# Optimization experiments

Measured on AMD Instinct MI355X. Metric: run time of the kernel, lower is better.

Reference implementation:

```python
import jax, jax.numpy as jnp
import numpy as np

B, VD, SD, CD, H, HEADS = 16384, 2048, 1024, 512, 256, 4
DH = H // HEADS
EPS = 1e-5


def layer_norm(x, g, b):
    m = jnp.mean(x, axis=-1, keepdims=True)
    v = jnp.var(x, axis=-1, keepdims=True)
    return (x - m) * jax.lax.rsqrt(v + EPS) * g + b


def setup_inputs() -> dict:
    key = jax.random.key(0)
    ks = jax.random.split(key, 16)
    sc = 0.02
    inp = {
        'fv': jax.random.normal(ks[0], (B, VD), jnp.float32),
        'fs': jax.random.normal(ks[1], (B, SD), jnp.float32),
        'fc': jax.random.normal(ks[2], (B, CD), jnp.float32),
        # projection linears + layernorms
        'Wv': jax.random.normal(ks[3], (H, VD), jnp.float32) * sc,
        'bv': jnp.zeros((H,), jnp.float32),
        'gv': jnp.ones((H,), jnp.float32), 'bev': jnp.zeros((H,), jnp.float32),
        'Ws': jax.random.normal(ks[4], (H, SD), jnp.float32) * sc,
        'bs': jnp.zeros((H,), jnp.float32),
        'gs': jnp.ones((H,), jnp.float32), 'bes': jnp.zeros((H,), jnp.float32),
        'Wc': jax.random.normal(ks[5], (H, CD), jnp.float32) * sc,
        'bc': jnp.zeros((H,), jnp.float32),
        'gc_': jnp.ones((H,), jnp.float32), 'bec': jnp.zeros((H,), jnp.float32),
        # MultiheadAttention packed in-proj and out-proj
        'in_w': jax.random.normal(ks[6], (3 * H, H), jnp.float32) * sc,
        'in_b': jnp.zeros((3 * H,), jnp.float32),
        'out_w': jax.random.normal(ks[7], (H, H), jnp.float32) * sc,
        'out_b': jnp.zeros((H,), jnp.float32),
        # post-attention layernorm
        'gn': jnp.ones((H,), jnp.float32), 'gb': jnp.zeros((H,), jnp.float32),
        # gating MLP: Linear(3H,64) -> GELU -> Linear(64,3) -> softmax
        'g1w': jax.random.normal(ks[8], (64, 3 * H), jnp.float32) * sc,
        'g1b': jnp.zeros((64,), jnp.float32),
        'g2w': jax.random.normal(ks[9], (3, 64), jnp.float32) * sc,
        'g2b': jnp.zeros((3,), jnp.float32),
    }
    return inp


def reference(fv, fs, fc, Wv, bv, gv, bev, Ws, bs, gs, bes, Wc, bc, gc_, bec,
              in_w, in_b, out_w, out_b, gn, gb, g1w, g1b, g2w, g2b):
    v = layer_norm(fv @ Wv.T + bv, gv, bev)   # [B,H]
    s = layer_norm(fs @ Ws.T + bs, gs, bes)
    c = layer_norm(fc @ Wc.T + bc, gc_, bec)
    stack = jnp.stack([v, s, c], axis=1)      # [B,3,H]

    # self-attention over seq=3 (eval mode: dropout off)
    qkv = stack @ in_w.T + in_b               # [B,3,3H]
    q, k, vv = jnp.split(qkv, 3, axis=-1)
    def heads(x):  # [B,3,H] -> [B,HEADS,3,DH]
        return x.reshape(B, 3, HEADS, DH).transpose(0, 2, 1, 3)
    q, k, vv = heads(q), heads(k), heads(vv)
    scores = jnp.einsum('bhqd,bhkd->bhqk', q, k) / jnp.sqrt(jnp.float32(DH))
    attn = jax.nn.softmax(scores, axis=-1)
    ctx = jnp.einsum('bhqk,bhkd->bhqd', attn, vv)
    ctx = ctx.transpose(0, 2, 1, 3).reshape(B, 3, H)
    attended = ctx @ out_w.T + out_b          # [B,3,H]

    attended = layer_norm(attended + stack, gn, gb)
    av, as_, ac = attended[:, 0], attended[:, 1], attended[:, 2]

    h1 = jax.nn.gelu(jnp.concatenate([av, as_, ac], axis=-1) @ g1w.T + g1b, approximate=False)
    gates = jax.nn.softmax(h1 @ g2w.T + g2b, axis=-1)  # [B,3]

    fused = gates[:, 0:1] * av + gates[:, 1:2] * as_ + gates[:, 2:3] * ac
    return (fused, gates)
```

## Files before the change

### kernel.cpp

```cpp
#include <hip/hip_runtime.h>
#include <math.h>


typedef unsigned short u16;
typedef __bf16 bf16x8 __attribute__((ext_vector_type(8)));
typedef float fx4 __attribute__((ext_vector_type(4)));

#define MFMA_BF16(A_, B_, C_) __builtin_amdgcn_mfma_f32_16x16x32_bf16((A_), (B_), (C_), 0, 0, 0)
#define WAIT_VM(N) asm volatile("s_waitcnt vmcnt(" #N ")" ::: "memory")

__device__ __forceinline__ float bf2f(u16 s) {
    union { float f; unsigned u; } c; c.u = ((unsigned)s) << 16; return c.f;
}
__device__ __forceinline__ u16 f2bf(float f) {
    union { float f; unsigned u; } c; c.f = f;
    return (u16)((c.u + 0x7fffu + ((c.u >> 16) & 1u)) >> 16);
}
__device__ __forceinline__ float bfpair_dot(unsigned a, unsigned b) {
    union { unsigned u; float f; } al, ah, bl, bh;
    al.u = a << 16; ah.u = a & 0xffff0000u;
    bl.u = b << 16; bh.u = b & 0xffff0000u;
    return al.f * bl.f + ah.f * bh.f;
}
__device__ __forceinline__ void gld16(void* l, const void* g) {
    __builtin_amdgcn_global_load_lds((const __attribute__((address_space(1))) void*)g,
                                     (__attribute__((address_space(3))) void*)l, 16, 0, 0);
}

__global__ __launch_bounds__(256) void cvt_w(const float* Wv, const float* Ws, const float* Wc,
                                             const float* inw, const float* outw, const float* g1w,
                                             u16* dst) {
    int idx = blockIdx.x * 256 + threadIdx.x;
    const float* src; int rel;
    if      (idx <  524288) { src = Wv;   rel = idx; }
    else if (idx <  786432) { src = Ws;   rel = idx -  524288; }
    else if (idx <  917504) { src = Wc;   rel = idx -  786432; }
    else if (idx < 1114112) { src = inw;  rel = idx -  917504; }
    else if (idx < 1179648) { src = outw; rel = idx - 1114112; }
    else                    { src = g1w;  rel = idx - 1179648; }
    dst[idx] = f2bf(src[rel]);
}

__global__ __launch_bounds__(256, 2) void gemm_ln(
    const float* fv, const float* fs, const float* fc,
    const u16* wWv, const u16* wWs, const u16* wWc,
    const float* bv, const float* gv, const float* bev,
    const float* bs, const float* gs, const float* bes,
    const float* bc, const float* gc_, const float* bec,
    u16* stack) {
    __shared__ alignas(16) char smem[76288];
    u16* sC = (u16*)smem;
    float* redS = (float*)(smem + 73728);
    float* redQ = (float*)(smem + 74752);
    float* mvS  = (float*)(smem + 75776);

    int bid = blockIdx.x;
    int slot, mblk;
    if (bid < 256)      { slot = 0; mblk = bid; }
    else if (bid < 512) { slot = 1; mblk = bid - 256; }
    else                { slot = 2; mblk = bid - 512; }

    const float* A; const u16* W; const float* bias; const float* gg; const float* be; int K;
    if (slot == 0)      { A = fv; W = wWv; bias = bv; gg = gv;  be = bev; K = 2048; }
    else if (slot == 1) { A = fs; W = wWs; bias = bs; gg = gs;  be = bes; K = 1024; }
    else                { A = fc; W = wWc; bias = bc; gg = gc_; be = bec; K = 512;  }

    int t = threadIdx.x, wv = t >> 6, ln = t & 63, q = ln >> 4, l15 = ln & 15;
    int m0 = mblk * 64;

    fx4 zero = {0.f, 0.f, 0.f, 0.f};
    fx4 acc[4][4];
    #pragma unroll
    for (int mi = 0; mi < 4; ++mi)
        #pragma unroll
        for (int ni = 0; ni < 4; ++ni) acc[mi][ni] = zero;

    int aR[2], aGC[2];
    #pragma unroll
    for (int i = 0; i < 2; ++i) {
        int d = wv * 128 + i * 64 + ln;
        aR[i] = d >> 3;
        aGC[i] = (d & 7) ^ (aR[i] & 7);
    }
    int bN[4], bKc[4];
    #pragma unroll
    for (int i = 0; i < 4; ++i) {
        int d = wv * 256 + i * 64 + ln;
        bN[i] = d >> 2;
        bKc[i] = (d & 3) ^ ((bN[i] >> 1) & 3);
    }

#define LN_ISSUE(ktile, bufoff)                                                   \
    {                                                                             \
        char* bA_ = smem + (bufoff);                                              \
        char* bB_ = bA_ + 8192;                                                   \
        _Pragma("unroll")                                                         \
        for (int i_ = 0; i_ < 2; ++i_)                                            \
            gld16(bA_ + (wv * 128 + i_ * 64) * 16,                                \
                  A + (size_t)(m0 + aR[i_]) * K + (ktile) * 32 + aGC[i_] * 4);    \
        _Pragma("unroll")                                                         \
        for (int i_ = 0; i_ < 4; ++i_)                                            \
            gld16(bB_ + (wv * 256 + i_ * 64) * 16,                                \
                  W + (size_t)bN[i_] * K + (ktile) * 32 + bKc[i_] * 8);           \
    }

    int niter = K >> 5;
    LN_ISSUE(0, 0);
    LN_ISSUE(1, 24576);
    int cb = 0;
    for (int kt = 0; kt < niter; ++kt) {
        if (kt + 1 < niter) { WAIT_VM(6); } else { WAIT_VM(0); }
        __builtin_amdgcn_sched_barrier(0);
        __builtin_amdgcn_s_barrier();
        __builtin_amdgcn_sched_barrier(0);
        int nb = cb + 2; if (nb >= 3) nb -= 3;
        if (kt + 2 < niter) LN_ISSUE(kt + 2, nb * 24576);

        const float* sAc = (const float*)(smem + cb * 24576);
        const u16*  sBc  = (const u16*)(smem + cb * 24576 + 8192);
        bf16x8 af[4], bfr[4];
        #pragma unroll
        for (int mi = 0; mi < 4; ++mi) {
            int r = mi * 16 + l15, s = r & 7;
            const float* rowp = sAc + r * 32;
            float4 c0 = *(const float4*)(rowp + ((2 * q) ^ s) * 4);
            float4 c1 = *(const float4*)(rowp + ((2 * q + 1) ^ s) * 4);
            af[mi][0] = (__bf16)c0.x; af[mi][1] = (__bf16)c0.y;
            af[mi][2] = (__bf16)c0.z; af[mi][3] = (__bf16)c0.w;
            af[mi][4] = (__bf16)c1.x; af[mi][5] = (__bf16)c1.y;
            af[mi][6] = (__bf16)c1.z; af[mi][7] = (__bf16)c1.w;
        }
        #pragma unroll
        for (int ni = 0; ni < 4; ++ni) {
            int n = wv * 64 + ni * 16 + l15;
            int ch = n * 4 + (q ^ ((n >> 1) & 3));
            bfr[ni] = *(const bf16x8*)(sBc + ch * 8);
        }
        __builtin_amdgcn_s_setprio(1);
        #pragma unroll
        for (int mi = 0; mi < 4; ++mi)
            #pragma unroll
            for (int ni = 0; ni < 4; ++ni)
                acc[mi][ni] = MFMA_BF16(af[mi], bfr[ni], acc[mi][ni]);
        __builtin_amdgcn_s_setprio(0);
        cb += 1; if (cb >= 3) cb -= 3;
    }
#undef LN_ISSUE

    float biasv[4], gvv[4], bevv[4];
    #pragma unroll
    for (int ni = 0; ni < 4; ++ni) {
        int col = wv * 64 + ni * 16 + l15;
        biasv[ni] = bias[col]; gvv[ni] = gg[col]; bevv[ni] = be[col];
    }
    #pragma unroll
    for (int mi = 0; mi < 4; ++mi)
        #pragma unroll
        for (int ni = 0; ni < 4; ++ni)
            #pragma unroll
            for (int r = 0; r < 4; ++r) acc[mi][ni][r] += biasv[ni];
    #pragma unroll
    for (int mi = 0; mi < 4; ++mi) {
        #pragma unroll
        for (int r = 0; r < 4; ++r) {
            float s = 0.f, qq = 0.f;
            #pragma unroll
            for (int ni = 0; ni < 4; ++ni) { float x = acc[mi][ni][r]; s += x; qq += x * x; }
            #pragma unroll
            for (int m = 1; m < 16; m <<= 1) { s += __shfl_xor(s, m, 64); qq += __shfl_xor(qq, m, 64); }
            if (l15 == 0) { int rho = mi * 16 + q * 4 + r; redS[rho * 4 + wv] = s; redQ[rho * 4 + wv] = qq; }
        }
    }
    __syncthreads();
    if (t < 64) {
        float s = redS[t * 4] + redS[t * 4 + 1] + redS[t * 4 + 2] + redS[t * 4 + 3];
        float qq = redQ[t * 4] + redQ[t * 4 + 1] + redQ[t * 4 + 2] + redQ[t * 4 + 3];
        float mean = s * (1.f / 256.f);
        float var = qq * (1.f / 256.f) - mean * mean;
        mvS[t * 2] = mean; mvS[t * 2 + 1] = rsqrtf(var + 1e-5f);
    }
    __syncthreads();
    #pragma unroll
    for (int mi = 0; mi < 4; ++mi) {
        #pragma unroll
        for (int r = 0; r < 4; ++r) {
            int rho = mi * 16 + q * 4 + r;
            float mean = mvS[rho * 2], rstd = mvS[rho * 2 + 1];
            #pragma unroll
            for (int ni = 0; ni < 4; ++ni) {
                int col = wv * 64 + ni * 16 + l15;
                float x = (acc[mi][ni][r] - mean) * rstd * gvv[ni] + bevv[ni];
                sC[rho * 256 + col] = f2bf(x);
            }
        }
    }
    __syncthreads();
    u16* outp = stack + (size_t)m0 * 768 + slot * 256;
    #pragma unroll
    for (int it = 0; it < 8; ++it) {
        int idx = t + it * 256;
        int row = idx >> 5, c = idx & 31;
        uint4 v = *(const uint4*)(sC + row * 256 + c * 8);
        *(uint4*)(outp + (size_t)row * 768 + c * 8) = v;
    }
}

__global__ __launch_bounds__(256, 3) void gemm_qkv(const u16* stack, const u16* W, const float* in_b,
                                                   u16* qkv) {
    __shared__ alignas(16) char smem[49152];
    u16* sC = (u16*)smem;

    int t = threadIdx.x, wv = t >> 6, ln = t & 63, q = ln >> 4, l15 = ln & 15;
    int n0 = blockIdx.x * 128, m0 = blockIdx.y * 128;
    int wr = wv >> 1, wc = wv & 1;

    fx4 zero = {0.f, 0.f, 0.f, 0.f};
    fx4 acc[4][4];
    #pragma unroll
    for (int mi = 0; mi < 4; ++mi)
        #pragma unroll
        for (int ni = 0; ni < 4; ++ni) acc[mi][ni] = zero;

    int sR[2], sKc[2];
    #pragma unroll
    for (int i = 0; i < 2; ++i) {
        int d = wv * 128 + i * 64 + ln;
        sR[i] = d >> 2;
        sKc[i] = (d & 3) ^ ((sR[i] >> 1) & 3);
    }

#define QK_ISSUE(ktile, bufoff)                                                         \
    {                                                                                   \
        char* bA_ = smem + (bufoff);                                                    \
        char* bB_ = bA_ + 8192;                                                         \
        _Pragma("unroll")                                                               \
        for (int i_ = 0; i_ < 2; ++i_) {                                                \
            gld16(bA_ + (wv * 128 + i_ * 64) * 16,                                      \
                  stack + (size_t)(m0 + sR[i_]) * 256 + (ktile) * 32 + sKc[i_] * 8);    \
            gld16(bB_ + (wv * 128 + i_ * 64) * 16,                                      \
                  W + (size_t)(n0 + sR[i_]) * 256 + (ktile) * 32 + sKc[i_] * 8);        \
        }                                                                               \
    }

    QK_ISSUE(0, 0);
    QK_ISSUE(1, 16384);
    int cb = 0;
    for (int kt = 0; kt < 8; ++kt) {
        if (kt < 7) { WAIT_VM(4); } else { WAIT_VM(0); }
        __builtin_amdgcn_sched_barrier(0);
        __builtin_amdgcn_s_barrier();
        __builtin_amdgcn_sched_barrier(0);
        int nb = cb + 2; if (nb >= 3) nb -= 3;
        if (kt + 2 < 8) QK_ISSUE(kt + 2, nb * 16384);

        const u16* sAc = (const u16*)(smem + cb * 16384);
        const u16* sBc = (const u16*)(smem + cb * 16384 + 8192);
        bf16x8 af[4], bfr[4];
        #pragma unroll
        for (int mi = 0; mi < 4; ++mi) {
            int r = wr * 64 + mi * 16 + l15;
            int ch = r * 4 + (q ^ ((r >> 1) & 3));
            af[mi] = *(const bf16x8*)(sAc + ch * 8);
        }
        #pragma unroll
        for (int ni = 0; ni < 4; ++ni) {
            int n = wc * 64 + ni * 16 + l15;
            int ch = n * 4 + (q ^ ((n >> 1) & 3));
            bfr[ni] = *(const bf16x8*)(sBc + ch * 8);
        }
        __builtin_amdgcn_s_setprio(1);
        #pragma unroll
        for (int mi = 0; mi < 4; ++mi)
            #pragma unroll
            for (int ni = 0; ni < 4; ++ni)
                acc[mi][ni] = MFMA_BF16(af[mi], bfr[ni], acc[mi][ni]);
        __builtin_amdgcn_s_setprio(0);
        cb += 1; if (cb >= 3) cb -= 3;
    }
#undef QK_ISSUE
    __syncthreads();

    float biasv[4];
    #pragma unroll
    for (int ni = 0; ni < 4; ++ni) biasv[ni] = in_b[n0 + wc * 64 + ni * 16 + l15];
    #pragma unroll
    for (int mi = 0; mi < 4; ++mi)
        #pragma unroll
        for (int ni = 0; ni < 4; ++ni)
            #pragma unroll
            for (int r = 0; r < 4; ++r) {
                int rl = wr * 64 + mi * 16 + q * 4 + r;
                int cl = wc * 64 + ni * 16 + l15;
                sC[rl * 128 + cl] = f2bf(acc[mi][ni][r] + biasv[ni]);
            }
    __syncthreads();
    #pragma unroll
    for (int it = 0; it < 8; ++it) {
        int idx = t + it * 256;
        int row = idx >> 4, c = idx & 15;
        uint4 v = *(const uint4*)(sC + row * 128 + c * 8);
        *(uint4*)(qkv + (size_t)(m0 + row) * 768 + n0 + c * 8) = v;
    }
}

__global__ __launch_bounds__(256) void attn_k(const u16* qkv, u16* ctx) {
    __shared__ alignas(16) char smem[38016];
    u16* qs = (u16*)smem;
    float* sS = (float*)(smem + 36864);

    int t = threadIdx.x, wv = t >> 6, ln = t & 63;
    size_t base = (size_t)blockIdx.x * 8 * 2304;
    #pragma unroll
    for (int i = 0; i < 9; ++i) {
        int d = wv * 576 + i * 64;
        gld16((char*)smem + (size_t)d * 16, qkv + base + (size_t)(d + ln) * 8);
    }
    __syncthreads();
    #pragma unroll
    for (int it = 0; it < 2; ++it) {
        int idx = t + it * 256;
        if (idx < 288) {
            int b = idx / 36, rem = idx % 36, h = rem / 9, pp = rem % 9, i = pp / 3, j = pp % 3;
            const u16* qp = qs + b * 2304 + i * 768 + h * 64;
            const u16* kp = qs + b * 2304 + j * 768 + 256 + h * 64;
            float acc = 0.f;
            #pragma unroll
            for (int c = 0; c < 8; ++c) {
                uint4 qa = *(const uint4*)(qp + c * 8);
                uint4 ka = *(const uint4*)(kp + c * 8);
                acc += bfpair_dot(qa.x, ka.x) + bfpair_dot(qa.y, ka.y) +
                       bfpair_dot(qa.z, ka.z) + bfpair_dot(qa.w, ka.w);
            }
            sS[idx] = acc * 0.125f;
        }
    }
    __syncthreads();
    if (t < 96) {
        int b3 = t * 3;
        float s0 = sS[b3], s1 = sS[b3 + 1], s2 = sS[b3 + 2];
        float m = fmaxf(s0, fmaxf(s1, s2));
        float e0 = __expf(s0 - m), e1 = __expf(s1 - m), e2 = __expf(s2 - m);
        float inv = 1.f / (e0 + e1 + e2);
        sS[b3] = e0 * inv; sS[b3 + 1] = e1 * inv; sS[b3 + 2] = e2 * inv;
    }
    __syncthreads();
    #pragma unroll
    for (int it = 0; it < 3; ++it) {
        int idx = t + it * 256;
        int b = idx / 96, rem = idx % 96, i = rem / 32, c = rem & 31, h = c >> 3;
        int pbase = b * 36 + h * 9 + i * 3;
        float o[8];
        #pragma unroll
        for (int e = 0; e < 8; ++e) o[e] = 0.f;
        #pragma unroll
        for (int j = 0; j < 3; ++j) {
            float p = sS[pbase + j];
            uint4 va = *(const uint4*)(qs + b * 2304 + j * 768 + 512 + c * 8);
            unsigned uu[4] = {va.x, va.y, va.z, va.w};
            #pragma unroll
            for (int pr = 0; pr < 4; ++pr) {
                union { unsigned u; float f; } lo, hi;
                lo.u = uu[pr] << 16; hi.u = uu[pr] & 0xffff0000u;
                o[2 * pr]     += p * lo.f;
                o[2 * pr + 1] += p * hi.f;
            }
        }
        union { u16 us[8]; uint4 v; } pk;
        #pragma unroll
        for (int e = 0; e < 8; ++e) pk.us[e] = f2bf(o[e]);
        *(uint4*)(ctx + (size_t)(blockIdx.x * 8 + b) * 768 + i * 256 + c * 8) = pk.v;
    }
}

__global__ __launch_bounds__(256) void outproj_k(
    const u16* ctx, const u16* W, const float* out_b, const u16* stack,
    const float* gn, const float* gb, const u16* g1w, const float* g1b,
    const float* g2w, const float* g2b, float* outF, float* outG) {
    __shared__ alignas(16) char smem[40960];
    u16* r1 = (u16*)smem;
    u16* sB = (u16*)(smem + 24576);
    float* redS = (float*)(smem + 24576);
    float* redQ = redS + 192;
    float* mvS = redQ + 192;
    float* h1S = (float*)(smem + 26624);
    float* lgS = (float*)(smem + 30720);
    float* gateS = lgS + 48;

    int t = threadIdx.x, wv = t >> 6, ln = t & 63, q = ln >> 4, l15 = ln & 15;
    int gr0 = blockIdx.x * 48, b0 = blockIdx.x * 16;

    #pragma unroll
    for (int i = 0; i < 6; ++i) {
        int d = wv * 384 + i * 64 + ln;
        int row = d >> 5, p = d & 31;
        int kc = p ^ (row & 7);
        gld16((char*)r1 + (wv * 384 + i * 64) * 16, ctx + (size_t)(gr0 + row) * 256 + kc * 8);
    }
    __syncthreads();

    fx4 zero = {0.f, 0.f, 0.f, 0.f};
    fx4 acc[3][4];
    #pragma unroll
    for (int mi = 0; mi < 3; ++mi)
        #pragma unroll
        for (int ni = 0; ni < 4; ++ni) acc[mi][ni] = zero;

    for (int kt = 0; kt < 8; ++kt) {
        #pragma unroll
        for (int i = 0; i < 4; ++i) {
            int d = wv * 256 + i * 64 + ln;
            int n = d >> 2, p = d & 3;
            int kc = p ^ ((n >> 1) & 3);
            gld16((char*)sB + (wv * 256 + i * 64) * 16, W + (size_t)n * 256 + kt * 32 + kc * 8);
        }
        __syncthreads();
        bf16x8 af[3], bfr[4];
        #pragma unroll
        for (int mi = 0; mi < 3; ++mi) {
            int row = mi * 16 + l15;
            int ch = row * 32 + ((kt * 4 + q) ^ (row & 7));
            af[mi] = *(const bf16x8*)(r1 + ch * 8);
        }
        #pragma unroll
        for (int ni = 0; ni < 4; ++ni) {
            int n = wv * 64 + ni * 16 + l15;
            int ch = n * 4 + (q ^ ((n >> 1) & 3));
            bfr[ni] = *(const bf16x8*)(sB + ch * 8);
        }
        #pragma unroll
        for (int mi = 0; mi < 3; ++mi)
            #pragma unroll
            for (int ni = 0; ni < 4; ++ni)
                acc[mi][ni] = MFMA_BF16(af[mi], bfr[ni], acc[mi][ni]);
        __syncthreads();
    }

    #pragma unroll
    for (int i = 0; i < 6; ++i) {
        int d = wv * 384 + i * 64 + ln;
        gld16((char*)r1 + (wv * 384 + i * 64) * 16, stack + (size_t)gr0 * 256 + (size_t)d * 8);
    }
    __syncthreads();

    float obv[4], gnv[4], gbv[4];
    #pragma unroll
    for (int ni = 0; ni < 4; ++ni) {
        int col = wv * 64 + ni * 16 + l15;
        obv[ni] = out_b[col]; gnv[ni] = gn[col]; gbv[ni] = gb[col];
    }
    #pragma unroll
    for (int mi = 0; mi < 3; ++mi)
        #pragma unroll
        for (int ni = 0; ni < 4; ++ni)
            #pragma unroll
            for (int r = 0; r < 4; ++r) {
                int rho = mi * 16 + q * 4 + r;
                int col = wv * 64 + ni * 16 + l15;
                acc[mi][ni][r] += obv[ni] + bf2f(r1[rho * 256 + col]);
            }
    #pragma unroll
    for (int mi = 0; mi < 3; ++mi) {
        #pragma unroll
        for (int r = 0; r < 4; ++r) {
            float s = 0.f, qq = 0.f;
            #pragma unroll
            for (int ni = 0; ni < 4; ++ni) { float x = acc[mi][ni][r]; s += x; qq += x * x; }
            #pragma unroll
            for (int m = 1; m < 16; m <<= 1) { s += __shfl_xor(s, m, 64); qq += __shfl_xor(qq, m, 64); }
            if (l15 == 0) { int rho = mi * 16 + q * 4 + r; redS[rho * 4 + wv] = s; redQ[rho * 4 + wv] = qq; }
        }
    }
    __syncthreads();
    if (t < 48) {
        float s = redS[t * 4] + redS[t * 4 + 1] + redS[t * 4 + 2] + redS[t * 4 + 3];
        float qq = redQ[t * 4] + redQ[t * 4 + 1] + redQ[t * 4 + 2] + redQ[t * 4 + 3];
        float mean = s * (1.f / 256.f);
        float var = qq * (1.f / 256.f) - mean * mean;
        mvS[t * 2] = mean; mvS[t * 2 + 1] = rsqrtf(var + 1e-5f);
    }
    __syncthreads();
    #pragma unroll
    for (int mi = 0; mi < 3; ++mi) {
        #pragma unroll
        for (int r = 0; r < 4; ++r) {
            int rho = mi * 16 + q * 4 + r;
            float mean = mvS[rho * 2], rstd = mvS[rho * 2 + 1];
            int bl = rho / 3, sl = rho - bl * 3;
            #pragma unroll
            for (int ni = 0; ni < 4; ++ni) {
                int col = wv * 64 + ni * 16 + l15;
                float x = (acc[mi][ni][r] - mean) * rstd * gnv[ni] + gbv[ni];
                int k = sl * 256 + col;
                int kidx = k >> 3, wn = k & 7;
                r1[(bl * 96 + (kidx ^ (bl & 7))) * 8 + wn] = f2bf(x);
            }
        }
    }
    __syncthreads();
    fx4 ag = zero;
    for (int kt = 0; kt < 24; ++kt) {
        int bl = l15;
        int kidx = kt * 4 + q;
        bf16x8 afr = *(const bf16x8*)(r1 + (bl * 96 + (kidx ^ (bl & 7))) * 8);
        int n = wv * 16 + l15;
        bf16x8 bfr2 = *(const bf16x8*)(g1w + (size_t)n * 768 + kt * 32 + q * 8);
        ag = MFMA_BF16(afr, bfr2, ag);
    }
    #pragma unroll
    for (int r = 0; r < 4; ++r) {
        int bl = q * 4 + r, n = wv * 16 + l15;
        float x = ag[r] + g1b[n];
        h1S[bl * 64 + n] = 0.5f * x * (1.f + erff(x * 0.70710678118f));
    }
    __syncthreads();
    if (t < 48) {
        int bl = t / 3, s = t - bl * 3;
        float a = g2b[s];
        #pragma unroll
        for (int k = 0; k < 64; ++k) a += h1S[bl * 64 + k] * g2w[s * 64 + k];
        lgS[t] = a;
    }
    __syncthreads();
    if (t < 48) {
        int bl = t / 3, s = t - bl * 3;
        float l0 = lgS[bl * 3], l1 = lgS[bl * 3 + 1], l2 = lgS[bl * 3 + 2];
        float m = fmaxf(l0, fmaxf(l1, l2));
        float e0 = __expf(l0 - m), e1 = __expf(l1 - m), e2 = __expf(l2 - m);
        float inv = 1.f / (e0 + e1 + e2);
        float gsel = ((s == 0) ? e0 : (s == 1) ? e1 : e2) * inv;
        gateS[t] = gsel;
        outG[(size_t)(b0 + bl) * 3 + s] = gsel;
    }
    __syncthreads();
    #pragma unroll
    for (int it = 0; it < 2; ++it) {
        int idx = t + it * 256;
        int b = idx >> 5, c = idx & 31;
        float g0 = gateS[b * 3], g1 = gateS[b * 3 + 1], g2 = gateS[b * 3 + 2];
        float o[8];
        #pragma unroll
        for (int e = 0; e < 8; ++e) o[e] = 0.f;
        #pragma unroll
        for (int s = 0; s < 3; ++s) {
            float gw = (s == 0) ? g0 : (s == 1) ? g1 : g2;
            int kidx = s * 32 + c;
            uint4 raw = *(const uint4*)(r1 + (b * 96 + (kidx ^ (b & 7))) * 8);
            unsigned uu[4] = {raw.x, raw.y, raw.z, raw.w};
            #pragma unroll
            for (int pr = 0; pr < 4; ++pr) {
                union { unsigned u; float f; } lo, hi;
                lo.u = uu[pr] << 16; hi.u = uu[pr] & 0xffff0000u;
                o[2 * pr]     += gw * lo.f;
                o[2 * pr + 1] += gw * hi.f;
            }
        }
        float* op = outF + (size_t)(b0 + b) * 256 + c * 8;
        float4 v0; v0.x = o[0]; v0.y = o[1]; v0.z = o[2]; v0.w = o[3];
        float4 v1; v1.x = o[4]; v1.y = o[5]; v1.z = o[6]; v1.w = o[7];
        *(float4*)op = v0;
        *(float4*)(op + 4) = v1;
    }
}

extern "C" void kernel_launch(void* const* d_in, const int* in_sizes, int n_in,
                              void* d_out, int out_size, void* d_ws, size_t ws_size,
                              hipStream_t stream) {
    (void)in_sizes; (void)n_in; (void)out_size; (void)ws_size;
    const float* fv   = (const float*)d_in[0];
    const float* fs   = (const float*)d_in[1];
    const float* fc   = (const float*)d_in[2];
    const float* Wv   = (const float*)d_in[3];
    const float* bv   = (const float*)d_in[4];
    const float* gv   = (const float*)d_in[5];
    const float* bev  = (const float*)d_in[6];
    const float* Ws   = (const float*)d_in[7];
    const float* bs   = (const float*)d_in[8];
    const float* gs   = (const float*)d_in[9];
    const float* bes  = (const float*)d_in[10];
    const float* Wc   = (const float*)d_in[11];
    const float* bc   = (const float*)d_in[12];
    const float* gc_  = (const float*)d_in[13];
    const float* bec  = (const float*)d_in[14];
    const float* in_w = (const float*)d_in[15];
    const float* in_b = (const float*)d_in[16];
    const float* out_w= (const float*)d_in[17];
    const float* out_b= (const float*)d_in[18];
    const float* gn   = (const float*)d_in[19];
    const float* gb   = (const float*)d_in[20];
    const float* g1w  = (const float*)d_in[21];
    const float* g1b  = (const float*)d_in[22];
    const float* g2w  = (const float*)d_in[23];
    const float* g2b  = (const float*)d_in[24];

    u16* w0    = (u16*)d_ws;
    u16* wWv   = w0;
    u16* wWs   = w0 + 524288;
    u16* wWc   = w0 + 786432;
    u16* wIn   = w0 + 917504;
    u16* wOut  = w0 + 1114112;
    u16* wG1   = w0 + 1179648;
    u16* stack = w0 + 1228800;
    u16* qkv   = w0 + 13811712;
    u16* ctx   = w0 + 51560448;
    float* outF = (float*)d_out;
    float* outG = outF + (size_t)16384 * 256;

    cvt_w<<<4800, 256, 0, stream>>>(Wv, Ws, Wc, in_w, out_w, g1w, w0);
    gemm_ln<<<768, 256, 0, stream>>>(fv, fs, fc, wWv, wWs, wWc,
                                     bv, gv, bev, bs, gs, bes, bc, gc_, bec, stack);
    gemm_qkv<<<dim3(6, 384), 256, 0, stream>>>(stack, wIn, in_b, qkv);
    attn_k<<<2048, 256, 0, stream>>>(qkv, ctx);
    outproj_k<<<1024, 256, 0, stream>>>(ctx, wOut, out_b, stack, gn, gb,
                                        wG1, g1b, g2w, g2b, outF, outG);
}
```

Baseline: 430.5 us.

## Restructure projection GEMM main loop: register-staged bf16 A tile, BK=64 double buffer

Replaces the triple-buffered, async global-to-LDS fp32 A loads with register prefetch of the next A tile. The tile is converted to bf16 once and stored into a padded LDS layout. K-tile depth doubles to 64 with a double-buffered B tile, and the per-iteration wait/barrier dance becomes a single __syncthreads. The aim is to halve A-tile LDS traffic, avoid repeated fp32-to-bf16 conversion per wave and halve barrier count. In exchange, LDS use grows and the launch-bounds occupancy hint of 2 blocks is dropped, which risks lower occupancy and less latency hiding.

```diff
diff --git a/kernel.cpp b/kernel.cpp
--- a/kernel.cpp
+++ b/kernel.cpp
@@ -41,18 +41,18 @@
     dst[idx] = f2bf(src[rel]);
 }
 
-__global__ __launch_bounds__(256, 2) void gemm_ln(
+__global__ __launch_bounds__(256) void gemm_ln(
     const float* fv, const float* fs, const float* fc,
     const u16* wWv, const u16* wWs, const u16* wWc,
     const float* bv, const float* gv, const float* bev,
     const float* bs, const float* gs, const float* bes,
     const float* bc, const float* gc_, const float* bec,
     u16* stack) {
-    __shared__ alignas(16) char smem[76288];
+    __shared__ alignas(16) char smem[86528];
     u16* sC = (u16*)smem;
-    float* redS = (float*)(smem + 73728);
-    float* redQ = (float*)(smem + 74752);
-    float* mvS  = (float*)(smem + 75776);
+    float* redS = (float*)(smem + 83968);
+    float* redQ = (float*)(smem + 84992);
+    float* mvS  = (float*)(smem + 86016);
 
     int bid = blockIdx.x;
     int slot, mblk;
@@ -75,77 +75,88 @@
         #pragma unroll
         for (int ni = 0; ni < 4; ++ni) acc[mi][ni] = zero;
 
-    int aR[2], aGC[2];
-    #pragma unroll
-    for (int i = 0; i < 2; ++i) {
-        int d = wv * 128 + i * 64 + ln;
-        aR[i] = d >> 3;
-        aGC[i] = (d & 7) ^ (aR[i] & 7);
-    }
-    int bN[4], bKc[4];
-    #pragma unroll
-    for (int i = 0; i < 4; ++i) {
-        int d = wv * 256 + i * 64 + ln;
-        bN[i] = d >> 2;
-        bKc[i] = (d & 3) ^ ((bN[i] >> 1) & 3);
-    }
-
-#define LN_ISSUE(ktile, bufoff)                                                   \
-    {                                                                             \
-        char* bA_ = smem + (bufoff);                                              \
-        char* bB_ = bA_ + 8192;                                                   \
-        _Pragma("unroll")                                                         \
-        for (int i_ = 0; i_ < 2; ++i_)                                            \
-            gld16(bA_ + (wv * 128 + i_ * 64) * 16,                                \
-                  A + (size_t)(m0 + aR[i_]) * K + (ktile) * 32 + aGC[i_] * 4);    \
-        _Pragma("unroll")                                                         \
-        for (int i_ = 0; i_ < 4; ++i_)                                            \
-            gld16(bB_ + (wv * 256 + i_ * 64) * 16,                                \
-                  W + (size_t)bN[i_] * K + (ktile) * 32 + bKc[i_] * 8);           \
-    }
-
-    int niter = K >> 5;
-    LN_ISSUE(0, 0);
-    LN_ISSUE(1, 24576);
-    int cb = 0;
+    int rowA = t >> 2, ca = t & 3;
+    const float* aBase = A + (size_t)(m0 + rowA) * K + ca * 16;
+    int sAwOff = rowA * 72 + ca * 16;
+
+    int bN[8], bKc[8], bDst[8];
+    #pragma unroll
+    for (int i = 0; i < 8; ++i) {
+        int d = i * 256 + t;
+        bN[i] = d >> 3;
+        bKc[i] = (d & 7) ^ (bN[i] & 7);
+        bDst[i] = d * 16;
+    }
+
+    int niter = K >> 6;
+
+    {
+        float4 f0 = *(const float4*)(aBase);
+        float4 f1 = *(const float4*)(aBase + 4);
+        float4 f2 = *(const float4*)(aBase + 8);
+        float4 f3 = *(const float4*)(aBase + 12);
+        #pragma unroll
+        for (int i = 0; i < 8; ++i)
+            gld16(smem + 18432 + bDst[i], W + (size_t)bN[i] * K + bKc[i] * 8);
+        union { u16 us[8]; uint4 v; } p0, p1;
+        p0.us[0] = f2bf(f0.x); p0.us[1] = f2bf(f0.y); p0.us[2] = f2bf(f0.z); p0.us[3] = f2bf(f0.w);
+        p0.us[4] = f2bf(f1.x); p0.us[5] = f2bf(f1.y); p0.us[6] = f2bf(f1.z); p0.us[7] = f2bf(f1.w);
+        p1.us[0] = f2bf(f2.x); p1.us[1] = f2bf(f2.y); p1.us[2] = f2bf(f2.z); p1.us[3] = f2bf(f2.w);
+        p1.us[4] = f2bf(f3.x); p1.us[5] = f2bf(f3.y); p1.us[6] = f2bf(f3.z); p1.us[7] = f2bf(f3.w);
+        *(uint4*)((u16*)smem + sAwOff) = p0.v;
+        *(uint4*)((u16*)smem + sAwOff + 8) = p1.v;
+    }
+    __syncthreads();
+
     for (int kt = 0; kt < niter; ++kt) {
-        if (kt + 1 < niter) { WAIT_VM(6); } else { WAIT_VM(0); }
-        __builtin_amdgcn_sched_barrier(0);
-        __builtin_amdgcn_s_barrier();
-        __builtin_amdgcn_sched_barrier(0);
-        int nb = cb + 2; if (nb >= 3) nb -= 3;
-        if (kt + 2 < niter) LN_ISSUE(kt + 2, nb * 24576);
-
-        const float* sAc = (const float*)(smem + cb * 24576);
-        const u16*  sBc  = (const u16*)(smem + cb * 24576 + 8192);
-        bf16x8 af[4], bfr[4];
-        #pragma unroll
-        for (int mi = 0; mi < 4; ++mi) {
-            int r = mi * 16 + l15, s = r & 7;
-            const float* rowp = sAc + r * 32;
-            float4 c0 = *(const float4*)(rowp + ((2 * q) ^ s) * 4);
-            float4 c1 = *(const float4*)(rowp + ((2 * q + 1) ^ s) * 4);
-            af[mi][0] = (__bf16)c0.x; af[mi][1] = (__bf16)c0.y;
-            af[mi][2] = (__bf16)c0.z; af[mi][3] = (__bf16)c0.w;
-            af[mi][4] = (__bf16)c1.x; af[mi][5] = (__bf16)c1.y;
-            af[mi][6] = (__bf16)c1.z; af[mi][7] = (__bf16)c1.w;
-        }
-        #pragma unroll
-        for (int ni = 0; ni < 4; ++ni) {
-            int n = wv * 64 + ni * 16 + l15;
-            int ch = n * 4 + (q ^ ((n >> 1) & 3));
-            bfr[ni] = *(const bf16x8*)(sBc + ch * 8);
-        }
-        __builtin_amdgcn_s_setprio(1);
-        #pragma unroll
-        for (int mi = 0; mi < 4; ++mi)
-            #pragma unroll
-            for (int ni = 0; ni < 4; ++ni)
-                acc[mi][ni] = MFMA_BF16(af[mi], bfr[ni], acc[mi][ni]);
-        __builtin_amdgcn_s_setprio(0);
-        cb += 1; if (cb >= 3) cb -= 3;
-    }
-#undef LN_ISSUE
+        int cur = kt & 1, nxt_b = (kt + 1) & 1;
+        u16* sAc = (u16*)(smem + cur * 9216);
+        u16* sBc = (u16*)(smem + 18432 + cur * 32768);
+        int has_next = (kt + 1) < niter;
+
+        float4 nf0, nf1, nf2, nf3;
+        if (has_next) {
+            nf0 = *(const float4*)(aBase + (kt + 1) * 64);
+            nf1 = *(const float4*)(aBase + (kt + 1) * 64 + 4);
+            nf2 = *(const float4*)(aBase + (kt + 1) * 64 + 8);
+            nf3 = *(const float4*)(aBase + (kt + 1) * 64 + 12);
+            char* sBn = smem + 18432 + nxt_b * 32768;
+            #pragma unroll
+            for (int i = 0; i < 8; ++i)
+                gld16(sBn + bDst[i], W + (size_t)bN[i] * K + (kt + 1) * 64 + bKc[i] * 8);
+        }
+
+        #pragma unroll
+        for (int kk = 0; kk < 2; ++kk) {
+            bf16x8 af[4], bfr[4];
+            #pragma unroll
+            for (int mi = 0; mi < 4; ++mi)
+                af[mi] = *(const bf16x8*)(sAc + (mi * 16 + l15) * 72 + kk * 32 + q * 8);
+            #pragma unroll
+            for (int ni = 0; ni < 4; ++ni) {
+                int n = wv * 64 + ni * 16 + l15;
+                int slotc = (kk * 4 + q) ^ (n & 7);
+                bfr[ni] = *(const bf16x8*)(sBc + (n * 8 + slotc) * 8);
+            }
+            #pragma unroll
+            for (int mi = 0; mi < 4; ++mi)
+                #pragma unroll
+                for (int ni = 0; ni < 4; ++ni)
+                    acc[mi][ni] = MFMA_BF16(af[mi], bfr[ni], acc[mi][ni]);
+        }
+
+        if (has_next) {
+            union { u16 us[8]; uint4 v; } p0, p1;
+            p0.us[0] = f2bf(nf0.x); p0.us[1] = f2bf(nf0.y); p0.us[2] = f2bf(nf0.z); p0.us[3] = f2bf(nf0.w);
+            p0.us[4] = f2bf(nf1.x); p0.us[5] = f2bf(nf1.y); p0.us[6] = f2bf(nf1.z); p0.us[7] = f2bf(nf1.w);
+            p1.us[0] = f2bf(nf2.x); p1.us[1] = f2bf(nf2.y); p1.us[2] = f2bf(nf2.z); p1.us[3] = f2bf(nf2.w);
+            p1.us[4] = f2bf(nf3.x); p1.us[5] = f2bf(nf3.y); p1.us[6] = f2bf(nf3.z); p1.us[7] = f2bf(nf3.w);
+            u16* sAn = (u16*)(smem + nxt_b * 9216);
+            *(uint4*)(sAn + sAwOff) = p0.v;
+            *(uint4*)(sAn + sAwOff + 8) = p1.v;
+        }
+        __syncthreads();
+    }
 
     float biasv[4], gvv[4], bevv[4];
     #pragma unroll
```

Measured after the change: 435.9 us. About the same (+1.2%).
